# Kernel tuning notes

Hardware: AMD Instinct MI355X
Metric: run time of the kernel (lower is better)

The kernel has to match this reference:

```python
import jax, jax.numpy as jnp
import numpy as np

NUM_BLOCKS = 8
HIDDEN_FACTOR = 1
LAMBD = 0.01
HARD_FRACTION = 1.0
SCALE = 0.02


def softshrink(v, lambd):
    return jnp.sign(v) * jnp.maximum(jnp.abs(v) - lambd, 0.0)


def setup_inputs() -> dict:
    key = jax.random.key(0)
    ks = jax.random.split(key, 5)
    B, H, W, C = 4, 128, 128, 768
    bs = C // NUM_BLOCKS
    x = jax.random.normal(ks[0], (B, H * W, C), dtype=jnp.float32)
    w1 = SCALE * jax.random.normal(ks[1], (2, NUM_BLOCKS, bs, bs * HIDDEN_FACTOR), dtype=jnp.float32)
    b1 = SCALE * jax.random.normal(ks[2], (2, NUM_BLOCKS, bs * HIDDEN_FACTOR), dtype=jnp.float32)
    w2 = SCALE * jax.random.normal(ks[3], (2, NUM_BLOCKS, bs * HIDDEN_FACTOR, bs), dtype=jnp.float32)
    b2 = SCALE * jax.random.normal(ks[4], (2, NUM_BLOCKS, bs), dtype=jnp.float32)
    return {"x": x, "w1": w1, "b1": b1, "w2": w2, "b2": b2, "H": H, "W": W}


def reference(x, w1, b1, w2, b2, H, W):
    B, N, C = x.shape
    bs = C // NUM_BLOCKS
    bias = x
    xf = x.astype(jnp.float32).reshape(B, H, W, C)
    x_fft = jnp.fft.rfft2(xf, axes=(1, 2), norm='ortho')  # [B,H,W//2+1,C]
    Wm = W // 2 + 1
    kept = max(1, int(Wm * HARD_FRACTION))
    xr = x_fft.real.reshape(B, H, Wm, NUM_BLOCKS, bs)
    xi = x_fft.imag.reshape(B, H, Wm, NUM_BLOCKS, bs)
    xr_k = xr[:, :, :kept]
    xi_k = xi[:, :, :kept]
    # block-diagonal complex layer 1 + relu
    o1r = jax.nn.relu(jnp.einsum('bhwni,nio->bhwno', xr_k, w1[0])
                      - jnp.einsum('bhwni,nio->bhwno', xi_k, w1[1]) + b1[0])
    o1i = jax.nn.relu(jnp.einsum('bhwni,nio->bhwno', xi_k, w1[0])
                      + jnp.einsum('bhwni,nio->bhwno', xr_k, w1[1]) + b1[1])
    # layer 2
    o2r = (jnp.einsum('bhwno,noi->bhwni', o1r, w2[0])
           - jnp.einsum('bhwno,noi->bhwni', o1i, w2[1]) + b2[0])
    o2i = (jnp.einsum('bhwno,noi->bhwni', o1i, w2[0])
           + jnp.einsum('bhwno,noi->bhwni', o1r, w2[1]) + b2[1])
    o2r = softshrink(o2r, LAMBD)
    o2i = softshrink(o2i, LAMBD)
    # zero-pad unkept modes (kept == Wm when HARD_FRACTION == 1.0)
    if kept < Wm:
        pad = [(0, 0), (0, 0), (0, Wm - kept), (0, 0), (0, 0)]
        o2r = jnp.pad(o2r, pad)
        o2i = jnp.pad(o2i, pad)
    x_c = (o2r + 1j * o2i).reshape(B, H, Wm, C)
    x_out = jnp.fft.irfft2(x_c, s=(H, W), axes=(1, 2), norm='ortho')
    return x_out.reshape(B, N, C).astype(bias.dtype) + bias
```

## Files before the change

### kernel.cpp

```cpp
#include <hip/hip_runtime.h>
#include <hip/hip_bf16.h>

#define BDIM 256
constexpr int Bc = 4, Hc = 128, Wcn = 128, Cc = 768, WM = 65, NB = 8, BS = 96;
constexpr int NROWS = Bc * WM * Hc;
constexpr size_t NSPEC = (size_t)NROWS * Cc;

typedef __attribute__((ext_vector_type(8))) _Float16 f16x8;
typedef __attribute__((ext_vector_type(4))) float f32x4;
typedef __attribute__((ext_vector_type(4))) unsigned int u32x4;

__device__ __forceinline__ unsigned short f2h(float f) {
    return __builtin_bit_cast(unsigned short, (_Float16)f);
}
__device__ __forceinline__ float h2f(unsigned short s) {
    return (float)__builtin_bit_cast(_Float16, s);
}
__device__ __forceinline__ void barx() {
    __builtin_amdgcn_sched_barrier(0);
    asm volatile("s_waitcnt lgkmcnt(0)" ::: "memory");
    __builtin_amdgcn_s_barrier();
    __builtin_amdgcn_sched_barrier(0);
    asm volatile("" ::: "memory");
}

__global__ __launch_bounds__(BDIM) void kprep(const float* __restrict__ w1,
                                              const float* __restrict__ w2,
                                              unsigned short* __restrict__ WTg) {
    int idx = blockIdx.x * BDIM + threadIdx.x;
    if (idx >= 294912) return;
    int k = idx % 96, n = (idx / 96) % 96, blk = (idx / 9216) % 8, mat = idx / 73728;
    const float* src = (mat < 2) ? w1 : w2;
    int q = mat & 1;
    WTg[idx] = f2h(src[(((size_t)q * 8 + blk) * 96 + k) * 96 + n]);
}

constexpr int K1PAD = 136;
__global__ __launch_bounds__(BDIM, 1) void k1m(const float* __restrict__ x,
                                               unsigned short* __restrict__ Rr,
                                               unsigned short* __restrict__ Ri) {
    __shared__ unsigned short Xt[64][K1PAD];
    const int tid = threadIdx.x;
    const int lane = tid & 63;
    const int wv = tid >> 6;
    const int b = blockIdx.x >> 7, h = blockIdx.x & 127;
    const float* xp = x + ((size_t)(b * 16384 + h * 128)) * 768;
    const size_t sbase = ((size_t)(b * WM) * 128 + h) * 768;

    f16x8 Af[2][4];
    {
        const int rlo = wv * 32 + (lane & 15);
        #pragma unroll
        for (int rf = 0; rf < 2; ++rf) {
            const int r = rlo + rf * 16;
            const int m = (r < 65) ? r : (r - 64);
            #pragma unroll
            for (int ks = 0; ks < 4; ++ks) {
                f16x8 v;
                #pragma unroll
                for (int j = 0; j < 8; ++j) {
                    int k = ks * 32 + ((lane >> 4) << 3) + j;
                    float th = (float)((m * k) & 127) * 0.04908738521234052f;
                    float s, c; __sincosf(th, &s, &c);
                    v[j] = (_Float16)(((r < 65) ? c : -s) * 0.0078125f);
                }
                Af[rf][ks] = v;
            }
        }
    }

    const int w = tid & 127, cg = tid >> 7;
    float4 pfv[8];
    #pragma unroll
    for (int q = 0; q < 8; ++q)
        pfv[q] = *(const float4*)(xp + (size_t)w * 768 + cg * 32 + q * 4);

    const int koff = (lane >> 4) << 3;

    for (int t = 0; t < 12; ++t) {
        #pragma unroll
        for (int q = 0; q < 8; ++q) {
            float4 v = pfv[q];
            int cb = cg * 32 + q * 4;
            Xt[cb + 0][w] = f2h(v.x);
            Xt[cb + 1][w] = f2h(v.y);
            Xt[cb + 2][w] = f2h(v.z);
            Xt[cb + 3][w] = f2h(v.w);
        }
        if (t < 11) {
            #pragma unroll
            for (int q = 0; q < 8; ++q)
                pfv[q] = *(const float4*)(xp + (size_t)w * 768 + (t + 1) * 64 + cg * 32 + q * 4);
        }
        barx();

        f32x4 acc[2][4];
        #pragma unroll
        for (int rf = 0; rf < 2; ++rf)
            #pragma unroll
            for (int cf = 0; cf < 4; ++cf)
                acc[rf][cf] = (f32x4){0, 0, 0, 0};
        #pragma unroll
        for (int ks = 0; ks < 4; ++ks) {
            #pragma unroll
            for (int cf = 0; cf < 4; ++cf) {
                const int cl = cf * 16 + (lane & 15);
                f16x8 Bf = *(const f16x8*)(&Xt[cl][ks * 32 + koff]);
                #pragma unroll
                for (int rf = 0; rf < 2; ++rf)
                    acc[rf][cf] = __builtin_amdgcn_mfma_f32_16x16x32_f16(Af[rf][ks], Bf, acc[rf][cf], 0, 0, 0);
            }
        }
        #pragma unroll
        for (int rf = 0; rf < 2; ++rf)
            #pragma unroll
            for (int cf = 0; cf < 4; ++cf) {
                int col = t * 64 + cf * 16 + (lane & 15);
                int r0 = wv * 32 + rf * 16 + ((lane >> 4) << 2);
                #pragma unroll
                for (int reg = 0; reg < 4; ++reg) {
                    int r = r0 + reg;
                    if (r < 65) {
                        Rr[sbase + (size_t)r * 98304 + col] = f2h(acc[rf][cf][reg]);
                        if (r == 0)  Ri[sbase + col] = 0;
                        if (r == 64) Ri[sbase + (size_t)64 * 98304 + col] = 0;
                    } else {
                        Ri[sbase + (size_t)(r - 64) * 98304 + col] = f2h(acc[rf][cf][reg]);
                    }
                }
            }
        barx();
    }
}

constexpr int KMT = 136;
__global__ __launch_bounds__(BDIM, 1) void kmid(unsigned short* __restrict__ Rr,
                                                unsigned short* __restrict__ Ri,
                                                const unsigned short* __restrict__ WTg,
                                                const float* __restrict__ b1,
                                                const float* __restrict__ b2) {
    extern __shared__ unsigned short lds[];
    unsigned short* Ct = lds;
    unsigned short* St = Ct + 128 * KMT;
    unsigned short* Xtr = St + 128 * KMT;
    unsigned short* Xti = Xtr + 96 * KMT;
    unsigned short* Y   = Xtr;

    const int tid = threadIdx.x;
    const int lane = tid & 63;
    const int wv = tid >> 6;
    const int s = blockIdx.x;
    const int blk = blockIdx.y;
    const size_t sbase = (size_t)s * 98304;

    const int hme = tid & 127, cgme = tid >> 7;
    u32x4 pfs[12];
    #pragma unroll
    for (int p = 0; p < 12; ++p) {
        const unsigned short* src = (p >= 6) ? Ri : Rr;
        int cg = (p % 6) * 2 + cgme;
        pfs[p] = *(const u32x4*)(src + sbase + (size_t)hme * 768 + blk * 96 + cg * 8);
    }

    for (int idx = tid; idx < 16384; idx += BDIM) {
        int h2 = idx >> 7, h = idx & 127;
        float th = (float)((h2 * h) & 127) * 0.04908738521234052f;
        float sv, cv; __sincosf(th, &sv, &cv);
        Ct[h2 * KMT + h] = f2h(cv);
        St[h2 * KMT + h] = f2h(sv);
    }

    const int n0 = wv * 48;
    float bias1[3], bias2[3];
    #pragma unroll
    for (int c = 0; c < 3; ++c) {
        int n = n0 + c * 16 + (lane & 15);
        bias1[c] = (n < 96) ? b1[blk * 96 + n] : b1[768 + blk * 96 + (n - 96)];
        bias2[c] = (n < 96) ? b2[blk * 96 + n] : b2[768 + blk * 96 + (n - 96)];
    }

    #pragma unroll
    for (int p = 0; p < 12; ++p) {
        unsigned short* dst = (p >= 6) ? Xti : Xtr;
        int cl = ((p % 6) * 2 + cgme) * 8;
        unsigned short tmp[8];
        *(u32x4*)&tmp[0] = pfs[p];
        #pragma unroll
        for (int j = 0; j < 8; ++j)
            dst[(cl + j) * KMT + hme] = tmp[j];
    }
    __syncthreads();

    const int arow0 = wv * 32 + (lane & 15);
    const int koff = (lane >> 4) << 3;
    const int rowoff = (lane >> 4) << 2;

    f32x4 accr[2][6], acci[2][6];
    #pragma unroll
    for (int rf = 0; rf < 2; ++rf)
        #pragma unroll
        for (int cf = 0; cf < 6; ++cf) {
            accr[rf][cf] = (f32x4){0, 0, 0, 0};
            acci[rf][cf] = (f32x4){0, 0, 0, 0};
        }
    #pragma unroll
    for (int ks = 0; ks < 4; ++ks) {
        f16x8 Cf[2], Sp[2], Sn[2];
        #pragma unroll
        for (int rf = 0; rf < 2; ++rf) {
            int off = (arow0 + rf * 16) * KMT + ks * 32 + koff;
            Cf[rf] = *(const f16x8*)(Ct + off);
            f16x8 sv = *(const f16x8*)(St + off);
            u32x4 u = __builtin_bit_cast(u32x4, sv);
            u ^= 0x80008000u;
            Sp[rf] = sv;
            Sn[rf] = __builtin_bit_cast(f16x8, u);
        }
        #pragma unroll
        for (int cf = 0; cf < 6; ++cf) {
            int boff = (cf * 16 + (lane & 15)) * KMT + ks * 32 + koff;
            f16x8 Br = *(const f16x8*)(Xtr + boff);
            f16x8 Bi = *(const f16x8*)(Xti + boff);
            #pragma unroll
            for (int rf = 0; rf < 2; ++rf) {
                accr[rf][cf] = __builtin_amdgcn_mfma_f32_16x16x32_f16(Cf[rf], Br, accr[rf][cf], 0, 0, 0);
                accr[rf][cf] = __builtin_amdgcn_mfma_f32_16x16x32_f16(Sp[rf], Bi, accr[rf][cf], 0, 0, 0);
                acci[rf][cf] = __builtin_amdgcn_mfma_f32_16x16x32_f16(Cf[rf], Bi, acci[rf][cf], 0, 0, 0);
                acci[rf][cf] = __builtin_amdgcn_mfma_f32_16x16x32_f16(Sn[rf], Br, acci[rf][cf], 0, 0, 0);
            }
        }
    }

    f16x8 Bf1[3][6], Bf2[3][6];
    #pragma unroll
    for (int c = 0; c < 3; ++c) {
        const int nq = (n0 + c * 16) < 96;
        const int nl = n0 + c * 16 + (lane & 15) - (nq ? 0 : 96);
        #pragma unroll
        for (int kit = 0; kit < 6; ++kit) {
            const int kq = kit < 3;
            const int kl = kit * 32 + koff - (kq ? 0 : 96);
            const int quad = kq ? (nq ? 0 : 1) : (nq ? 1 : 0);
            const bool flip = (!kq) && nq;
            {
                f16x8 v = *(const f16x8*)(WTg + ((size_t)(quad * 8 + blk) * 96 + nl) * 96 + kl);
                if (flip) { u32x4 u = __builtin_bit_cast(u32x4, v); u ^= 0x80008000u; v = __builtin_bit_cast(f16x8, u); }
                Bf1[c][kit] = v;
            }
            {
                f16x8 v = *(const f16x8*)(WTg + ((size_t)((2 + quad) * 8 + blk) * 96 + nl) * 96 + kl);
                if (flip) { u32x4 u = __builtin_bit_cast(u32x4, v); u ^= 0x80008000u; v = __builtin_bit_cast(f16x8, u); }
                Bf2[c][kit] = v;
            }
        }
    }

    barx();
    #pragma unroll
    for (int rf = 0; rf < 2; ++rf)
        #pragma unroll
        for (int cf = 0; cf < 6; ++cf) {
            int c = cf * 16 + (lane & 15);
            #pragma unroll
            for (int reg = 0; reg < 4; ++reg) {
                int row = wv * 32 + rf * 16 + rowoff + reg;
                Y[row * 200 + c]      = f2h(accr[rf][cf][reg]);
                Y[row * 200 + 96 + c] = f2h(acci[rf][cf][reg]);
            }
        }
    barx();

    const unsigned short* Xl = Y + (lane & 15) * 200 + ((lane >> 4) << 3);
    f32x4 acc[8][3];
    #pragma unroll
    for (int r = 0; r < 8; ++r)
        #pragma unroll
        for (int c = 0; c < 3; ++c)
            acc[r][c] = (f32x4){bias1[c], bias1[c], bias1[c], bias1[c]};
    #pragma unroll
    for (int kit = 0; kit < 6; ++kit) {
        f16x8 A[8];
        #pragma unroll
        for (int r = 0; r < 8; ++r)
            A[r] = *(const f16x8*)(Xl + r * 3200 + kit * 32);
        #pragma unroll
        for (int r = 0; r < 8; ++r)
            #pragma unroll
            for (int c = 0; c < 3; ++c)
                acc[r][c] = __builtin_amdgcn_mfma_f32_16x16x32_f16(A[r], Bf1[c][kit], acc[r][c], 0, 0, 0);
    }
    __syncthreads();
    #pragma unroll
    for (int r = 0; r < 8; ++r)
        #pragma unroll
        for (int c = 0; c < 3; ++c) {
            int ncol = n0 + c * 16 + (lane & 15);
            #pragma unroll
            for (int reg = 0; reg < 4; ++reg) {
                int row = r * 16 + rowoff + reg;
                Y[row * 200 + ncol] = f2h(fmaxf(acc[r][c][reg], 0.f));
            }
        }
    __syncthreads();

    #pragma unroll
    for (int r = 0; r < 8; ++r)
        #pragma unroll
        for (int c = 0; c < 3; ++c)
            acc[r][c] = (f32x4){bias2[c], bias2[c], bias2[c], bias2[c]};
    #pragma unroll
    for (int kit = 0; kit < 6; ++kit) {
        f16x8 A[8];
        #pragma unroll
        for (int r = 0; r < 8; ++r)
            A[r] = *(const f16x8*)(Xl + r * 3200 + kit * 32);
        #pragma unroll
        for (int r = 0; r < 8; ++r)
            #pragma unroll
            for (int c = 0; c < 3; ++c)
                acc[r][c] = __builtin_amdgcn_mfma_f32_16x16x32_f16(A[r], Bf2[c][kit], acc[r][c], 0, 0, 0);
    }
    __syncthreads();
    #pragma unroll
    for (int r = 0; r < 8; ++r)
        #pragma unroll
        for (int c = 0; c < 3; ++c) {
            int ncol = n0 + c * 16 + (lane & 15);
            unsigned short* dst = (ncol < 96) ? Xtr : Xti;
            int cc = (ncol < 96) ? ncol : ncol - 96;
            #pragma unroll
            for (int reg = 0; reg < 4; ++reg) {
                int row = r * 16 + rowoff + reg;
                float v = acc[r][c][reg];
                v = (v > 0.01f) ? v - 0.01f : ((v < -0.01f) ? v + 0.01f : 0.f);
                dst[cc * KMT + row] = f2h(v);
            }
        }
    __syncthreads();

    #pragma unroll
    for (int rf = 0; rf < 2; ++rf)
        #pragma unroll
        for (int cf = 0; cf < 6; ++cf) {
            accr[rf][cf] = (f32x4){0, 0, 0, 0};
            acci[rf][cf] = (f32x4){0, 0, 0, 0};
        }
    #pragma unroll
    for (int ks = 0; ks < 4; ++ks) {
        f16x8 Cf[2], Sp[2], Sn[2];
        #pragma unroll
        for (int rf = 0; rf < 2; ++rf) {
            int off = (arow0 + rf * 16) * KMT + ks * 32 + koff;
            Cf[rf] = *(const f16x8*)(Ct + off);
            f16x8 sv = *(const f16x8*)(St + off);
            u32x4 u = __builtin_bit_cast(u32x4, sv);
            u ^= 0x80008000u;
            Sp[rf] = sv;
            Sn[rf] = __builtin_bit_cast(f16x8, u);
        }
        #pragma unroll
        for (int cf = 0; cf < 6; ++cf) {
            int boff = (cf * 16 + (lane & 15)) * KMT + ks * 32 + koff;
            f16x8 Br = *(const f16x8*)(Xtr + boff);
            f16x8 Bi = *(const f16x8*)(Xti + boff);
            #pragma unroll
            for (int rf = 0; rf < 2; ++rf) {
                accr[rf][cf] = __builtin_amdgcn_mfma_f32_16x16x32_f16(Cf[rf], Br, accr[rf][cf], 0, 0, 0);
                accr[rf][cf] = __builtin_amdgcn_mfma_f32_16x16x32_f16(Sn[rf], Bi, accr[rf][cf], 0, 0, 0);
                acci[rf][cf] = __builtin_amdgcn_mfma_f32_16x16x32_f16(Cf[rf], Bi, acci[rf][cf], 0, 0, 0);
                acci[rf][cf] = __builtin_amdgcn_mfma_f32_16x16x32_f16(Sp[rf], Br, acci[rf][cf], 0, 0, 0);
            }
        }
    }
    #pragma unroll
    for (int rf = 0; rf < 2; ++rf)
        #pragma unroll
        for (int cf = 0; cf < 6; ++cf) {
            int c = blk * 96 + cf * 16 + (lane & 15);
            int h0 = wv * 32 + rf * 16 + rowoff;
            #pragma unroll
            for (int reg = 0; reg < 4; ++reg) {
                size_t a = sbase + (size_t)(h0 + reg) * 768 + c;
                Rr[a] = f2h(accr[rf][cf][reg]);
                Ri[a] = f2h(acci[rf][cf][reg]);
            }
        }
}

constexpr int K5PAD = 104;
__global__ __launch_bounds__(BDIM, 1) void k5m(const unsigned short* __restrict__ Rr,
                                               const unsigned short* __restrict__ Ri,
                                               const float* __restrict__ x,
                                               float* __restrict__ out) {
    __shared__ unsigned short Xt[2][64][K5PAD];
    const int tid = threadIdx.x;
    const int lane = tid & 63;
    const int wv = tid >> 6;
    const int b = blockIdx.x >> 7, h = blockIdx.x & 127;
    const size_t rowbase = ((size_t)(b * WM) * 128 + h) * 768;
    const size_t obase = ((size_t)(b * 16384 + h * 128)) * 768;

    f16x8 Ca[2][3], Sa[2][3];
    {
        const int wrow_lo = wv * 32 + (lane & 15);
        #pragma unroll
        for (int rf = 0; rf < 2; ++rf) {
            const int wrow = wrow_lo + rf * 16;
            #pragma unroll
            for (int ks = 0; ks < 3; ++ks) {
                f16x8 cv, sv;
                #pragma unroll
                for (int j = 0; j < 8; ++j) {
                    int wm = ks * 32 + ((lane >> 4) << 3) + j;
                    float alpha = (wm > 64) ? 0.f : ((wm == 0 || wm == 64) ? 1.f : 2.f);
                    float th = (float)((wrow * wm) & 127) * 0.04908738521234052f;
                    float s, c; __sincosf(th, &s, &c);
                    cv[j] = (_Float16)(alpha * 0.0078125f * c);
                    sv[j] = (_Float16)(-alpha * 0.0078125f * s);
                }
                Ca[rf][ks] = cv;
                Sa[rf][ks] = sv;
            }
        }
    }

    for (int idx = tid; idx < 2 * 64 * 31; idx += BDIM) {
        int plane = idx / (64 * 31), rem = idx % (64 * 31);
        int cl = rem / 31, wm = 65 + rem % 31;
        Xt[plane][cl][wm] = 0;
    }

    unsigned short pfs[4][8], pfn[8];
    #pragma unroll
    for (int i = 0; i < 4; ++i) {
        const unsigned short* src = (i >> 1) ? Ri : Rr;
        int grp = (i & 1) * 4 + wv;
        *(u32x4*)&pfs[i][0] = *(const u32x4*)(src + rowbase + (size_t)lane * 98304 + grp * 8);
    }
    if (tid < 16) {
        const unsigned short* src = (tid >> 3) ? Ri : Rr;
        *(u32x4*)&pfn[0] = *(const u32x4*)(src + rowbase + (size_t)64 * 98304 + (tid & 7) * 8);
    }

    for (int t = 0; t < 12; ++t) {
        #pragma unroll
        for (int i = 0; i < 4; ++i) {
            int plane = i >> 1, grp = (i & 1) * 4 + wv;
            #pragma unroll
            for (int j = 0; j < 8; ++j)
                Xt[plane][grp * 8 + j][lane] = pfs[i][j];
        }
        if (tid < 16) {
            int plane = tid >> 3, grp = tid & 7;
            #pragma unroll
            for (int j = 0; j < 8; ++j)
                Xt[plane][grp * 8 + j][64] = pfn[j];
        }
        if (t < 11) {
            #pragma unroll
            for (int i = 0; i < 4; ++i) {
                const unsigned short* src = (i >> 1) ? Ri : Rr;
                int grp = (i & 1) * 4 + wv;
                *(u32x4*)&pfs[i][0] = *(const u32x4*)(src + rowbase + (size_t)lane * 98304 + (t + 1) * 64 + grp * 8);
            }
            if (tid < 16) {
                const unsigned short* src = (tid >> 3) ? Ri : Rr;
                *(u32x4*)&pfn[0] = *(const u32x4*)(src + rowbase + (size_t)64 * 98304 + (t + 1) * 64 + (tid & 7) * 8);
            }
        }
        barx();

        f32x4 acc[2][4];
        #pragma unroll
        for (int rf = 0; rf < 2; ++rf)
            #pragma unroll
            for (int cf = 0; cf < 4; ++cf)
                acc[rf][cf] = (f32x4){0, 0, 0, 0};
        const int koff = (lane >> 4) << 3;
        #pragma unroll
        for (int ks = 0; ks < 3; ++ks) {
            #pragma unroll
            for (int cf = 0; cf < 4; ++cf) {
                const int cl = cf * 16 + (lane & 15);
                f16x8 Br = *(const f16x8*)(&Xt[0][cl][ks * 32 + koff]);
                f16x8 Bi = *(const f16x8*)(&Xt[1][cl][ks * 32 + koff]);
                #pragma unroll
                for (int rf = 0; rf < 2; ++rf) {
                    acc[rf][cf] = __builtin_amdgcn_mfma_f32_16x16x32_f16(Ca[rf][ks], Br, acc[rf][cf], 0, 0, 0);
                    acc[rf][cf] = __builtin_amdgcn_mfma_f32_16x16x32_f16(Sa[rf][ks], Bi, acc[rf][cf], 0, 0, 0);
                }
            }
        }
        #pragma unroll
        for (int rf = 0; rf < 2; ++rf)
            #pragma unroll
            for (int cf = 0; cf < 4; ++cf) {
                int col = t * 64 + cf * 16 + (lane & 15);
                int row0 = wv * 32 + rf * 16 + ((lane >> 4) << 2);
                #pragma unroll
                for (int reg = 0; reg < 4; ++reg) {
                    size_t a = obase + (size_t)(row0 + reg) * 768 + col;
                    out[a] = acc[rf][cf][reg] + x[a];
                }
            }
        barx();
    }
}

extern "C" void kernel_launch(void* const* d_in, const int* in_sizes, int n_in,
                              void* d_out, int out_size, void* d_ws, size_t ws_size,
                              hipStream_t stream) {
    const float* x  = (const float*)d_in[0];
    const float* w1 = (const float*)d_in[1];
    const float* b1 = (const float*)d_in[2];
    const float* w2 = (const float*)d_in[3];
    const float* b2 = (const float*)d_in[4];
    float* out = (float*)d_out;

    unsigned short* Rr = (unsigned short*)d_ws;
    unsigned short* Ri = Rr + NSPEC;
    unsigned short* WTg = Ri + NSPEC;

    const size_t kmlds = (size_t)(2 * 128 * KMT + 2 * 96 * KMT) * 2;

    kprep<<<dim3(1152), BDIM, 0, stream>>>(w1, w2, WTg);
    k1m<<<dim3(512), BDIM, 0, stream>>>(x, Rr, Ri);
    kmid<<<dim3(260, 8), BDIM, kmlds, stream>>>(Rr, Ri, WTg, b1, b2);
    k5m<<<dim3(512), BDIM, 0, stream>>>(Rr, Ri, x, out);
}
```

Measured before the change: 358.6 us.

## Use 512 threads in kmid and split rows across eight waves

The middle kernel now runs with 8 waves instead of 4. Each wave handles 16 rows of the H-DFT instead of 32, and the channel-MLP work is split across a 2x4 grid of waves (row half by column quarter). This halves the per-thread accumulator and fragment registers and gives more latency hiding inside each block. The cost is duplicated weight fragment loads per wave (Bf1/Bf2 are loaded by both row halves) and more barrier participants.

```diff
diff --git a/kernel.cpp b/kernel.cpp
--- a/kernel.cpp
+++ b/kernel.cpp
@@ -2,6 +2,7 @@
 #include <hip/hip_bf16.h>
 
 #define BDIM 256
+#define BDIM2 512
 constexpr int Bc = 4, Hc = 128, Wcn = 128, Cc = 768, WM = 65, NB = 8, BS = 96;
 constexpr int NROWS = Bc * WM * Hc;
 constexpr size_t NSPEC = (size_t)NROWS * Cc;
@@ -134,11 +135,11 @@
 }
 
 constexpr int KMT = 136;
-__global__ __launch_bounds__(BDIM, 1) void kmid(unsigned short* __restrict__ Rr,
-                                                unsigned short* __restrict__ Ri,
-                                                const unsigned short* __restrict__ WTg,
-                                                const float* __restrict__ b1,
-                                                const float* __restrict__ b2) {
+__global__ __launch_bounds__(BDIM2, 1) void kmid(unsigned short* __restrict__ Rr,
+                                                 unsigned short* __restrict__ Ri,
+                                                 const unsigned short* __restrict__ WTg,
+                                                 const float* __restrict__ b1,
+                                                 const float* __restrict__ b2) {
     extern __shared__ unsigned short lds[];
     unsigned short* Ct = lds;
     unsigned short* St = Ct + 128 * KMT;
@@ -149,20 +150,21 @@
     const int tid = threadIdx.x;
     const int lane = tid & 63;
     const int wv = tid >> 6;
-    const int s = blockIdx.x;
+    const int wm = wv >> 2;
+    const int wn = wv & 3;
     const int blk = blockIdx.y;
-    const size_t sbase = (size_t)s * 98304;
+    const size_t sbase = (size_t)blockIdx.x * 98304;
 
     const int hme = tid & 127, cgme = tid >> 7;
-    u32x4 pfs[12];
-    #pragma unroll
-    for (int p = 0; p < 12; ++p) {
-        const unsigned short* src = (p >= 6) ? Ri : Rr;
-        int cg = (p % 6) * 2 + cgme;
+    u32x4 pfs[6];
+    #pragma unroll
+    for (int p = 0; p < 6; ++p) {
+        const unsigned short* src = (p >= 3) ? Ri : Rr;
+        int cg = (p % 3) * 4 + cgme;
         pfs[p] = *(const u32x4*)(src + sbase + (size_t)hme * 768 + blk * 96 + cg * 8);
     }
 
-    for (int idx = tid; idx < 16384; idx += BDIM) {
+    for (int idx = tid; idx < 16384; idx += BDIM2) {
         int h2 = idx >> 7, h = idx & 127;
         float th = (float)((h2 * h) & 127) * 0.04908738521234052f;
         float sv, cv; __sincosf(th, &sv, &cv);
@@ -170,7 +172,7 @@
         St[h2 * KMT + h] = f2h(sv);
     }
 
-    const int n0 = wv * 48;
+    const int n0 = wn * 48;
     float bias1[3], bias2[3];
     #pragma unroll
     for (int c = 0; c < 3; ++c) {
@@ -180,9 +182,9 @@
     }
 
     #pragma unroll
-    for (int p = 0; p < 12; ++p) {
-        unsigned short* dst = (p >= 6) ? Xti : Xtr;
-        int cl = ((p % 6) * 2 + cgme) * 8;
+    for (int p = 0; p < 6; ++p) {
+        unsigned short* dst = (p >= 3) ? Xti : Xtr;
+        int cl = ((p % 3) * 4 + cgme) * 8;
         unsigned short tmp[8];
         *(u32x4*)&tmp[0] = pfs[p];
         #pragma unroll
@@ -191,43 +193,33 @@
     }
     __syncthreads();
 
-    const int arow0 = wv * 32 + (lane & 15);
+    const int arow = wv * 16 + (lane & 15);
     const int koff = (lane >> 4) << 3;
     const int rowoff = (lane >> 4) << 2;
 
-    f32x4 accr[2][6], acci[2][6];
-    #pragma unroll
-    for (int rf = 0; rf < 2; ++rf)
-        #pragma unroll
-        for (int cf = 0; cf < 6; ++cf) {
-            accr[rf][cf] = (f32x4){0, 0, 0, 0};
-            acci[rf][cf] = (f32x4){0, 0, 0, 0};
-        }
+    f32x4 accr[6], acci[6];
+    #pragma unroll
+    for (int cf = 0; cf < 6; ++cf) {
+        accr[cf] = (f32x4){0, 0, 0, 0};
+        acci[cf] = (f32x4){0, 0, 0, 0};
+    }
     #pragma unroll
     for (int ks = 0; ks < 4; ++ks) {
-        f16x8 Cf[2], Sp[2], Sn[2];
-        #pragma unroll
-        for (int rf = 0; rf < 2; ++rf) {
-            int off = (arow0 + rf * 16) * KMT + ks * 32 + koff;
-            Cf[rf] = *(const f16x8*)(Ct + off);
-            f16x8 sv = *(const f16x8*)(St + off);
-            u32x4 u = __builtin_bit_cast(u32x4, sv);
-            u ^= 0x80008000u;
-            Sp[rf] = sv;
-            Sn[rf] = __builtin_bit_cast(f16x8, u);
-        }
+        int off = arow * KMT + ks * 32 + koff;
+        f16x8 Cf = *(const f16x8*)(Ct + off);
+        f16x8 Sp = *(const f16x8*)(St + off);
+        u32x4 u = __builtin_bit_cast(u32x4, Sp);
+        u ^= 0x80008000u;
+        f16x8 Sn = __builtin_bit_cast(f16x8, u);
         #pragma unroll
         for (int cf = 0; cf < 6; ++cf) {
             int boff = (cf * 16 + (lane & 15)) * KMT + ks * 32 + koff;
             f16x8 Br = *(const f16x8*)(Xtr + boff);
             f16x8 Bi = *(const f16x8*)(Xti + boff);
-            #pragma unroll
-            for (int rf = 0; rf < 2; ++rf) {
-                accr[rf][cf] = __builtin_amdgcn_mfma_f32_16x16x32_f16(Cf[rf], Br, accr[rf][cf], 0, 0, 0);
-                accr[rf][cf] = __builtin_amdgcn_mfma_f32_16x16x32_f16(Sp[rf], Bi, accr[rf][cf], 0, 0, 0);
-                acci[rf][cf] = __builtin_amdgcn_mfma_f32_16x16x32_f16(Cf[rf], Bi, acci[rf][cf], 0, 0, 0);
-                acci[rf][cf] = __builtin_amdgcn_mfma_f32_16x16x32_f16(Sn[rf], Br, acci[rf][cf], 0, 0, 0);
-            }
+            accr[cf] = __builtin_amdgcn_mfma_f32_16x16x32_f16(Cf, Br, accr[cf], 0, 0, 0);
+            accr[cf] = __builtin_amdgcn_mfma_f32_16x16x32_f16(Sp, Bi, accr[cf], 0, 0, 0);
+            acci[cf] = __builtin_amdgcn_mfma_f32_16x16x32_f16(Cf, Bi, acci[cf], 0, 0, 0);
+            acci[cf] = __builtin_amdgcn_mfma_f32_16x16x32_f16(Sn, Br, acci[cf], 0, 0, 0);
         }
     }
 
@@ -257,72 +249,70 @@
 
     barx();
     #pragma unroll
-    for (int rf = 0; rf < 2; ++rf)
-        #pragma unroll
-        for (int cf = 0; cf < 6; ++cf) {
-            int c = cf * 16 + (lane & 15);
-            #pragma unroll
-            for (int reg = 0; reg < 4; ++reg) {
-                int row = wv * 32 + rf * 16 + rowoff + reg;
-                Y[row * 200 + c]      = f2h(accr[rf][cf][reg]);
-                Y[row * 200 + 96 + c] = f2h(acci[rf][cf][reg]);
-            }
-        }
+    for (int cf = 0; cf < 6; ++cf) {
+        int c = cf * 16 + (lane & 15);
+        #pragma unroll
+        for (int reg = 0; reg < 4; ++reg) {
+            int row = wv * 16 + rowoff + reg;
+            Y[row * 200 + c]      = f2h(accr[cf][reg]);
+            Y[row * 200 + 96 + c] = f2h(acci[cf][reg]);
+        }
+    }
     barx();
 
-    const unsigned short* Xl = Y + (lane & 15) * 200 + ((lane >> 4) << 3);
-    f32x4 acc[8][3];
-    #pragma unroll
-    for (int r = 0; r < 8; ++r)
+    const unsigned short* Xl = Y + (wm * 64 + (lane & 15)) * 200 + koff;
+    f32x4 acc[4][3];
+    #pragma unroll
+    for (int r = 0; r < 4; ++r)
         #pragma unroll
         for (int c = 0; c < 3; ++c)
             acc[r][c] = (f32x4){bias1[c], bias1[c], bias1[c], bias1[c]};
     #pragma unroll
     for (int kit = 0; kit < 6; ++kit) {
-        f16x8 A[8];
-        #pragma unroll
-        for (int r = 0; r < 8; ++r)
+        f16x8 A[4];
+        #pragma unroll
+        for (int r = 0; r < 4; ++r)
             A[r] = *(const f16x8*)(Xl + r * 3200 + kit * 32);
         #pragma unroll
-        for (int r = 0; r < 8; ++r)
+        for (int r = 0; r < 4; ++r)
             #pragma unroll
             for (int c = 0; c < 3; ++c)
                 acc[r][c] = __builtin_amdgcn_mfma_f32_16x16x32_f16(A[r], Bf1[c][kit], acc[r][c], 0, 0, 0);
     }
     __syncthreads();
     #pragma unroll
-    for (int r = 0; r < 8; ++r)
+    for (int r = 0; r < 4; ++r)
         #pragma unroll
         for (int c = 0; c < 3; ++c) {
             int ncol = n0 + c * 16 + (lane & 15);
             #pragma unroll
             for (int reg = 0; reg < 4; ++reg) {
-                int row = r * 16 + rowoff + reg;
+                int row = wm * 64 + r * 16 + rowoff + reg;
                 Y[row * 200 + ncol] = f2h(fmaxf(acc[r][c][reg], 0.f));
             }
         }
     __syncthreads();
 
     #pragma unroll
-    for (int r = 0; r < 8; ++r)
+    for (int r = 0; r < 4; ++r)
         #pragma unroll
         for (int c = 0; c < 3; ++c)
             acc[r][c] = (f32x4){bias2[c], bias2[c], bias2[c], bias2[c]};
     #pragma unroll
     for (int kit = 0; kit < 6; ++kit) {
-        f16x8 A[8];
-        #pragma unroll
-        for (int r = 0; r < 8; ++r)
+        f16x8 A[4];
+        #pragma unroll
+        for (int r = 0; r < 4; ++r)
             A[r] = *(const f16x8*)(Xl + r * 3200 + kit * 32);
         #pragma unroll
-        for (int r = 0; r < 8; ++r)
+        for (int r = 0; r < 4; ++r)
             #pragma unroll
             for (int c = 0; c < 3; ++c)
                 acc[r][c] = __builtin_amdgcn_mfma_f32_16x16x32_f16(A[r], Bf2[c][kit], acc[r][c], 0, 0, 0);
     }
     __syncthreads();
     #pragma unroll
-    for (int r = 0; r < 8; ++r)
+    for (int r = 0; r < 4; ++r)
         #pragma unroll
         for (int c = 0; c < 3; ++c) {
             int ncol = n0 + c * 16 + (lane & 15);
@@ -330,7 +320,7 @@
             int cc = (ncol < 96) ? ncol : ncol - 96;
             #pragma unroll
             for (int reg = 0; reg < 4; ++reg) {
-                int row = r * 16 + rowoff + reg;
+                int row = wm * 64 + r * 16 + rowoff + reg;
                 float v = acc[r][c][reg];
                 v = (v > 0.01f) ? v - 0.01f : ((v < -0.01f) ? v + 0.01f : 0.f);
                 dst[cc * KMT + row] = f2h(v);
@@ -339,52 +329,40 @@
     __syncthreads();
 
     #pragma unroll
-    for (int rf = 0; rf < 2; ++rf)
-        #pragma unroll
-        for (int cf = 0; cf < 6; ++cf) {
-            accr[rf][cf] = (f32x4){0, 0, 0, 0};
-            acci[rf][cf] = (f32x4){0, 0, 0, 0};
-        }
+    for (int cf = 0; cf < 6; ++cf) {
+        accr[cf] = (f32x4){0, 0, 0, 0};
+        acci[cf] = (f32x4){0, 0, 0, 0};
+    }
     #pragma unroll
     for (int ks = 0; ks < 4; ++ks) {
-        f16x8 Cf[2], Sp[2], Sn[2];
-        #pragma unroll
-        for (int rf = 0; rf < 2; ++rf) {
-            int off = (arow0 + rf * 16) * KMT + ks * 32 + koff;
-            Cf[rf] = *(const f16x8*)(Ct + off);
-            f16x8 sv = *(const f16x8*)(St + off);
-            u32x4 u = __builtin_bit_cast(u32x4, sv);
-            u ^= 0x80008000u;
-            Sp[rf] = sv;
-            Sn[rf] = __builtin_bit_cast(f16x8, u);
-        }
+        int off = arow * KMT + ks * 32 + koff;
+        f16x8 Cf = *(const f16x8*)(Ct + off);
+        f16x8 Sp = *(const f16x8*)(St + off);
+        u32x4 u = __builtin_bit_cast(u32x4, Sp);
+        u ^= 0x80008000u;
+        f16x8 Sn = __builtin_bit_cast(f16x8, u);
         #pragma unroll
         for (int cf = 0; cf < 6; ++cf) {
             int boff = (cf * 16 + (lane & 15)) * KMT + ks * 32 + koff;
             f16x8 Br = *(const f16x8*)(Xtr + boff);
             f16x8 Bi = *(const f16x8*)(Xti + boff);
-            #pragma unroll
-            for (int rf = 0; rf < 2; ++rf) {
-                accr[rf][cf] = __builtin_amdgcn_mfma_f32_16x16x32_f16(Cf[rf], Br, accr[rf][cf], 0, 0, 0);
-                accr[rf][cf] = __builtin_amdgcn_mfma_f32_16x16x32_f16(Sn[rf], Bi, accr[rf][cf], 0, 0, 0);
-                acci[rf][cf] = __builtin_amdgcn_mfma_f32_16x16x32_f16(Cf[rf], Bi, acci[rf][cf], 0, 0, 0);
-                acci[rf][cf] = __builtin_amdgcn_mfma_f32_16x16x32_f16(Sp[rf], Br, acci[rf][cf], 0, 0, 0);
-            }
-        }
-    }
-    #pragma unroll
-    for (int rf = 0; rf < 2; ++rf)
-        #pragma unroll
-        for (int cf = 0; cf < 6; ++cf) {
-            int c = blk * 96 + cf * 16 + (lane & 15);
-            int h0 = wv * 32 + rf * 16 + rowoff;
-            #pragma unroll
-            for (int reg = 0; reg < 4; ++reg) {
-                size_t a = sbase + (size_t)(h0 + reg) * 768 + c;
-                Rr[a] = f2h(accr[rf][cf][reg]);
-                Ri[a] = f2h(acci[rf][cf][reg]);
-            }
-        }
+            accr[cf] = __builtin_amdgcn_mfma_f32_16x16x32_f16(Cf, Br, accr[cf], 0, 0, 0);
+            accr[cf] = __builtin_amdgcn_mfma_f32_16x16x32_f16(Sn, Bi, accr[cf], 0, 0, 0);
+            acci[cf] = __builtin_amdgcn_mfma_f32_16x16x32_f16(Cf, Bi, acci[cf], 0, 0, 0);
+            acci[cf] = __builtin_amdgcn_mfma_f32_16x16x32_f16(Sp, Br, acci[cf], 0, 0, 0);
+        }
+    }
+    #pragma unroll
+    for (int cf = 0; cf < 6; ++cf) {
+        int c = blk * 96 + cf * 16 + (lane & 15);
+        int h0 = wv * 16 + rowoff;
+        #pragma unroll
+        for (int reg = 0; reg < 4; ++reg) {
+            size_t a = sbase + (size_t)(h0 + reg) * 768 + c;
+            Rr[a] = f2h(accr[cf][reg]);
+            Ri[a] = f2h(acci[cf][reg]);
+        }
+    }
 }
 
 constexpr int K5PAD = 104;
@@ -525,6 +503,6 @@
 
     kprep<<<dim3(1152), BDIM, 0, stream>>>(w1, w2, WTg);
     k1m<<<dim3(512), BDIM, 0, stream>>>(x, Rr, Ri);
-    kmid<<<dim3(260, 8), BDIM, kmlds, stream>>>(Rr, Ri, WTg, b1, b2);
+    kmid<<<dim3(260, 8), BDIM2, kmlds, stream>>>(Rr, Ri, WTg, b1, b2);
     k5m<<<dim3(512), BDIM, 0, stream>>>(Rr, Ri, x, out);
 }
```

Result: slower. 394.3 us (+10.0%).

## Compute DFT twiddles in registers in kmid and drop LDS twiddle tables

Applied to the files above, without the earlier changes.

Each lane now computes the cos/sin twiddle fragments it needs for the H-axis DFT directly in registers with __sincosf, instead of filling 128x136 cos and sin tables in LDS and reading them back. This cuts kmid's dynamic LDS from about 122 KB to about 52 KB. Launch bounds are raised to 2 blocks per CU to exploit the freed LDS. The cost is more transcendental ALU work per lane, because the table computed once per block is now recomputed in both DFT phases, plus more live registers under a tighter register budget.

```diff
diff --git a/kernel.cpp b/kernel.cpp
--- a/kernel.cpp
+++ b/kernel.cpp
@@ -134,24 +134,21 @@
 }
 
 constexpr int KMT = 136;
-__global__ __launch_bounds__(BDIM, 1) void kmid(unsigned short* __restrict__ Rr,
+__global__ __launch_bounds__(BDIM, 2) void kmid(unsigned short* __restrict__ Rr,
                                                 unsigned short* __restrict__ Ri,
                                                 const unsigned short* __restrict__ WTg,
                                                 const float* __restrict__ b1,
                                                 const float* __restrict__ b2) {
     extern __shared__ unsigned short lds[];
-    unsigned short* Ct = lds;
-    unsigned short* St = Ct + 128 * KMT;
-    unsigned short* Xtr = St + 128 * KMT;
+    unsigned short* Xtr = lds;
     unsigned short* Xti = Xtr + 96 * KMT;
-    unsigned short* Y   = Xtr;
+    unsigned short* Y   = lds;
 
     const int tid = threadIdx.x;
     const int lane = tid & 63;
     const int wv = tid >> 6;
-    const int s = blockIdx.x;
     const int blk = blockIdx.y;
-    const size_t sbase = (size_t)s * 98304;
+    const size_t sbase = (size_t)blockIdx.x * 98304;
 
     const int hme = tid & 127, cgme = tid >> 7;
     u32x4 pfs[12];
@@ -162,14 +159,6 @@
         pfs[p] = *(const u32x4*)(src + sbase + (size_t)hme * 768 + blk * 96 + cg * 8);
     }
 
-    for (int idx = tid; idx < 16384; idx += BDIM) {
-        int h2 = idx >> 7, h = idx & 127;
-        float th = (float)((h2 * h) & 127) * 0.04908738521234052f;
-        float sv, cv; __sincosf(th, &sv, &cv);
-        Ct[h2 * KMT + h] = f2h(cv);
-        St[h2 * KMT + h] = f2h(sv);
-    }
-
     const int n0 = wv * 48;
     float bias1[3], bias2[3];
     #pragma unroll
@@ -178,6 +167,10 @@
         bias1[c] = (n < 96) ? b1[blk * 96 + n] : b1[768 + blk * 96 + (n - 96)];
         bias2[c] = (n < 96) ? b2[blk * 96 + n] : b2[768 + blk * 96 + (n - 96)];
     }
+
+    const int arow0 = wv * 32 + (lane & 15);
+    const int koff = (lane >> 4) << 3;
+    const int rowoff = (lane >> 4) << 2;
 
     #pragma unroll
     for (int p = 0; p < 12; ++p) {
@@ -191,10 +184,6 @@
     }
     __syncthreads();
 
-    const int arow0 = wv * 32 + (lane & 15);
-    const int koff = (lane >> 4) << 3;
-    const int rowoff = (lane >> 4) << 2;
-
     f32x4 accr[2][6], acci[2][6];
     #pragma unroll
     for (int rf = 0; rf < 2; ++rf)
@@ -203,30 +192,47 @@
             accr[rf][cf] = (f32x4){0, 0, 0, 0};
             acci[rf][cf] = (f32x4){0, 0, 0, 0};
         }
-    #pragma unroll
-    for (int ks = 0; ks < 4; ++ks) {
-        f16x8 Cf[2], Sp[2], Sn[2];
+    {
+        f16x8 Ca[2][4], Sa[2][4];
         #pragma unroll
         for (int rf = 0; rf < 2; ++rf) {
-            int off = (arow0 + rf * 16) * KMT + ks * 32 + koff;
-            Cf[rf] = *(const f16x8*)(Ct + off);
-            f16x8 sv = *(const f16x8*)(St + off);
-            u32x4 u = __builtin_bit_cast(u32x4, sv);
-            u ^= 0x80008000u;
-            Sp[rf] = sv;
-            Sn[rf] = __builtin_bit_cast(f16x8, u);
-        }
-        #pragma unroll
-        for (int cf = 0; cf < 6; ++cf) {
-            int boff = (cf * 16 + (lane & 15)) * KMT + ks * 32 + koff;
-            f16x8 Br = *(const f16x8*)(Xtr + boff);
-            f16x8 Bi = *(const f16x8*)(Xti + boff);
+            const int r = arow0 + rf * 16;
+            #pragma unroll
+            for (int ks = 0; ks < 4; ++ks) {
+                f16x8 cv, sv;
+                #pragma unroll
+                for (int j = 0; j < 8; ++j) {
+                    int k = ks * 32 + koff + j;
+                    float th = (float)((r * k) & 127) * 0.04908738521234052f;
+                    float s, c; __sincosf(th, &s, &c);
+                    cv[j] = (_Float16)c;
+                    sv[j] = (_Float16)s;
+                }
+                Ca[rf][ks] = cv;
+                Sa[rf][ks] = sv;
+            }
+        }
+        #pragma unroll
+        for (int ks = 0; ks < 4; ++ks) {
+            f16x8 Sn[2];
             #pragma unroll
             for (int rf = 0; rf < 2; ++rf) {
-                accr[rf][cf] = __builtin_amdgcn_mfma_f32_16x16x32_f16(Cf[rf], Br, accr[rf][cf], 0, 0, 0);
-                accr[rf][cf] = __builtin_amdgcn_mfma_f32_16x16x32_f16(Sp[rf], Bi, accr[rf][cf], 0, 0, 0);
-                acci[rf][cf] = __builtin_amdgcn_mfma_f32_16x16x32_f16(Cf[rf], Bi, acci[rf][cf], 0, 0, 0);
-                acci[rf][cf] = __builtin_amdgcn_mfma_f32_16x16x32_f16(Sn[rf], Br, acci[rf][cf], 0, 0, 0);
+                u32x4 u = __builtin_bit_cast(u32x4, Sa[rf][ks]);
+                u ^= 0x80008000u;
+                Sn[rf] = __builtin_bit_cast(f16x8, u);
+            }
+            #pragma unroll
+            for (int cf = 0; cf < 6; ++cf) {
+                int boff = (cf * 16 + (lane & 15)) * KMT + ks * 32 + koff;
+                f16x8 Br = *(const f16x8*)(Xtr + boff);
+                f16x8 Bi = *(const f16x8*)(Xti + boff);
+                #pragma unroll
+                for (int rf = 0; rf < 2; ++rf) {
+                    accr[rf][cf] = __builtin_amdgcn_mfma_f32_16x16x32_f16(Ca[rf][ks], Br, accr[rf][cf], 0, 0, 0);
+                    accr[rf][cf] = __builtin_amdgcn_mfma_f32_16x16x32_f16(Sa[rf][ks], Bi, accr[rf][cf], 0, 0, 0);
+                    acci[rf][cf] = __builtin_amdgcn_mfma_f32_16x16x32_f16(Ca[rf][ks], Bi, acci[rf][cf], 0, 0, 0);
+                    acci[rf][cf] = __builtin_amdgcn_mfma_f32_16x16x32_f16(Sn[rf], Br, acci[rf][cf], 0, 0, 0);
+                }
             }
         }
     }
@@ -270,7 +276,7 @@
         }
     barx();
 
-    const unsigned short* Xl = Y + (lane & 15) * 200 + ((lane >> 4) << 3);
+    const unsigned short* Xl = Y + (lane & 15) * 200 + koff;
     f32x4 acc[8][3];
     #pragma unroll
     for (int r = 0; r < 8; ++r)
@@ -345,30 +351,47 @@
             accr[rf][cf] = (f32x4){0, 0, 0, 0};
             acci[rf][cf] = (f32x4){0, 0, 0, 0};
         }
-    #pragma unroll
-    for (int ks = 0; ks < 4; ++ks) {
-        f16x8 Cf[2], Sp[2], Sn[2];
+    {
+        f16x8 Ca[2][4], Sa[2][4];
         #pragma unroll
         for (int rf = 0; rf < 2; ++rf) {
-            int off = (arow0 + rf * 16) * KMT + ks * 32 + koff;
-            Cf[rf] = *(const f16x8*)(Ct + off);
-            f16x8 sv = *(const f16x8*)(St + off);
-            u32x4 u = __builtin_bit_cast(u32x4, sv);
-            u ^= 0x80008000u;
-            Sp[rf] = sv;
-            Sn[rf] = __builtin_bit_cast(f16x8, u);
-        }
-        #pragma unroll
-        for (int cf = 0; cf < 6; ++cf) {
-            int boff = (cf * 16 + (lane & 15)) * KMT + ks * 32 + koff;
-            f16x8 Br = *(const f16x8*)(Xtr + boff);
-            f16x8 Bi = *(const f16x8*)(Xti + boff);
+            const int r = arow0 + rf * 16;
+            #pragma unroll
+            for (int ks = 0; ks < 4; ++ks) {
+                f16x8 cv, sv;
+                #pragma unroll
+                for (int j = 0; j < 8; ++j) {
+                    int k = ks * 32 + koff + j;
+                    float th = (float)((r * k) & 127) * 0.04908738521234052f;
+                    float s, c; __sincosf(th, &s, &c);
+                    cv[j] = (_Float16)c;
+                    sv[j] = (_Float16)s;
+                }
+                Ca[rf][ks] = cv;
+                Sa[rf][ks] = sv;
+            }
+        }
+        #pragma unroll
+        for (int ks = 0; ks < 4; ++ks) {
+            f16x8 Sn[2];
             #pragma unroll
             for (int rf = 0; rf < 2; ++rf) {
-                accr[rf][cf] = __builtin_amdgcn_mfma_f32_16x16x32_f16(Cf[rf], Br, accr[rf][cf], 0, 0, 0);
-                accr[rf][cf] = __builtin_amdgcn_mfma_f32_16x16x32_f16(Sn[rf], Bi, accr[rf][cf], 0, 0, 0);
-                acci[rf][cf] = __builtin_amdgcn_mfma_f32_16x16x32_f16(Cf[rf], Bi, acci[rf][cf], 0, 0, 0);
-                acci[rf][cf] = __builtin_amdgcn_mfma_f32_16x16x32_f16(Sp[rf], Br, acci[rf][cf], 0, 0, 0);
+                u32x4 u = __builtin_bit_cast(u32x4, Sa[rf][ks]);
+                u ^= 0x80008000u;
+                Sn[rf] = __builtin_bit_cast(f16x8, u);
+            }
+            #pragma unroll
+            for (int cf = 0; cf < 6; ++cf) {
+                int boff = (cf * 16 + (lane & 15)) * KMT + ks * 32 + koff;
+                f16x8 Br = *(const f16x8*)(Xtr + boff);
+                f16x8 Bi = *(const f16x8*)(Xti + boff);
+                #pragma unroll
+                for (int rf = 0; rf < 2; ++rf) {
+                    accr[rf][cf] = __builtin_amdgcn_mfma_f32_16x16x32_f16(Ca[rf][ks], Br, accr[rf][cf], 0, 0, 0);
+                    accr[rf][cf] = __builtin_amdgcn_mfma_f32_16x16x32_f16(Sn[rf], Bi, accr[rf][cf], 0, 0, 0);
+                    acci[rf][cf] = __builtin_amdgcn_mfma_f32_16x16x32_f16(Ca[rf][ks], Bi, acci[rf][cf], 0, 0, 0);
+                    acci[rf][cf] = __builtin_amdgcn_mfma_f32_16x16x32_f16(Sa[rf][ks], Br, acci[rf][cf], 0, 0, 0);
+                }
             }
         }
     }
@@ -521,7 +544,7 @@
     unsigned short* Ri = Rr + NSPEC;
     unsigned short* WTg = Ri + NSPEC;
 
-    const size_t kmlds = (size_t)(2 * 128 * KMT + 2 * 96 * KMT) * 2;
+    const size_t kmlds = (size_t)(2 * 96 * KMT) * 2;
 
     kprep<<<dim3(1152), BDIM, 0, stream>>>(w1, w2, WTg);
     k1m<<<dim3(512), BDIM, 0, stream>>>(x, Rr, Ri);
```

Result: slower. 392.9 us (+9.6%).
